# Performance work log

Measured on AMD Instinct MI355X. Metric: run time of the kernel, lower is better.

Reference implementation:

```python
import jax, jax.numpy as jnp
import numpy as np

B, S, HID = 1, 2048, 2880
NH, NKV, D = 64, 8, 64
G = NH // NKV          # GQA group size = 8
SW = 128               # sliding window
SCALE = D ** -0.5
NEG = -1e30


def rotate_half(x):
    h = x.shape[-1] // 2
    return jnp.concatenate([-x[..., h:], x[..., :h]], axis=-1)


def setup_inputs() -> dict:
    key = jax.random.key(0)
    ks = jax.random.split(key, 11)
    hidden_states = jax.random.normal(ks[0], (B, S, HID), dtype=jnp.float32)
    # RoPE tables [S, D]
    inv_freq = 1.0 / (10000.0 ** (np.arange(0, D, 2, dtype=np.float32) / D))
    freqs = np.arange(S, dtype=np.float32)[:, None] * inv_freq[None, :]
    emb = np.concatenate([freqs, freqs], axis=-1)
    cos = jnp.asarray(np.cos(emb), dtype=jnp.float32)
    sin = jnp.asarray(np.sin(emb), dtype=jnp.float32)
    std = 0.02
    wq = jax.random.normal(ks[1], (HID, NH * D), dtype=jnp.float32) * std
    bq = jax.random.normal(ks[2], (NH * D,), dtype=jnp.float32) * std
    wk = jax.random.normal(ks[3], (HID, NKV * D), dtype=jnp.float32) * std
    bk = jax.random.normal(ks[4], (NKV * D,), dtype=jnp.float32) * std
    wv = jax.random.normal(ks[5], (HID, NKV * D), dtype=jnp.float32) * std
    bv = jax.random.normal(ks[6], (NKV * D,), dtype=jnp.float32) * std
    wo = jax.random.normal(ks[7], (NH * D, HID), dtype=jnp.float32) * std
    bo = jax.random.normal(ks[8], (HID,), dtype=jnp.float32) * std
    sinks = jax.random.normal(ks[9], (NH,), dtype=jnp.float32)
    return dict(hidden_states=hidden_states, cos=cos, sin=sin, wq=wq, bq=bq,
                wk=wk, bk=bk, wv=wv, bv=bv, wo=wo, bo=bo, sinks=sinks)


def reference(hidden_states, cos, sin, wq, bq, wk, bk, wv, bv, wo, bo, sinks):
    b, s, _ = hidden_states.shape
    q = (hidden_states @ wq + bq).reshape(b, s, NH, D)
    k = (hidden_states @ wk + bk).reshape(b, s, NKV, D)
    v = (hidden_states @ wv + bv).reshape(b, s, NKV, D)
    # RoPE (rotate-half), cos/sin broadcast over batch and heads
    c = cos[None, :, None, :]
    si = sin[None, :, None, :]
    q = q * c + rotate_half(q) * si
    k = k * c + rotate_half(k) * si
    # GQA: [b, s, kv, g, d]
    qg = q.reshape(b, s, NKV, G, D)
    # scores [b, kv, g, q, s]
    scores = jnp.einsum('bqkgd,bskd->bkgqs', qg, k) * SCALE
    i = jnp.arange(s)
    allowed = (i[:, None] >= i[None, :]) & (i[:, None] - i[None, :] < SW)
    scores = jnp.where(allowed[None, None, None], scores, NEG)
    # sink softmax: per-head learnable logit added to the denominator only
    sink = sinks.reshape(NKV, G)[None, :, :, None]            # [1, kv, g, 1]
    m = jnp.maximum(scores.max(axis=-1), sink)                # [b, kv, g, q]
    e = jnp.exp(scores - m[..., None])
    denom = e.sum(axis=-1) + jnp.exp(sink - m)                # sink absorbs mass
    p = e / denom[..., None]
    attn = jnp.einsum('bkgqs,bskd->bqkgd', p, v).reshape(b, s, NH * D)
    return attn @ wo + bo
```

## Files before the change

kernel.cpp:

```cpp
#include <hip/hip_runtime.h>
#include <hip/hip_bf16.h>
#include <stdint.h>

#define S_LEN 2048
#define HID 2880
#define NH 64
#define NKV 8
#define HD 64
#define NQ (NH * HD)
#define NKVD (NKV * HD)
#define SCALE 0.125f

typedef unsigned short u16;
typedef __attribute__((ext_vector_type(8))) short short8;
typedef __attribute__((ext_vector_type(4))) float floatx4;

__device__ __forceinline__ u16 f2bf(float f) {
  union { float f; unsigned u; } x; x.f = f;
  unsigned r = x.u + 0x7fffu + ((x.u >> 16) & 1u);
  return (u16)(r >> 16);
}

__device__ __forceinline__ int xcd_swz(int orig, int nwg) {
  int q = nwg >> 3, r = nwg & 7, xcd = orig & 7, lid = orig >> 3;
  return (xcd < r ? xcd * (q + 1) : r * (q + 1) + (xcd - r) * q) + lid;
}

__device__ __forceinline__ void gl2lds16(const void* g, void* l) {
  __builtin_amdgcn_global_load_lds(
      (__attribute__((address_space(1))) unsigned int*)(uintptr_t)g,
      (__attribute__((address_space(3))) unsigned int*)(unsigned int)(uintptr_t)l,
      16, 0, 0);
}

__global__ void k_pre(const float* __restrict__ hs, u16* __restrict__ hsb,
                      const float* __restrict__ wq, const float* __restrict__ wk,
                      const float* __restrict__ wv, const float* __restrict__ wo,
                      u16* __restrict__ wqt, u16* __restrict__ wkt,
                      u16* __restrict__ wvt, u16* __restrict__ wot) {
  int b = blockIdx.x;
  const int ncv = (S_LEN * HID / 4) / 256;
  if (b < ncv) {
    int i = b * 256 + threadIdx.x;
    float4 v = ((const float4*)hs)[i];
    ushort4 o;
    o.x = f2bf(v.x); o.y = f2bf(v.y); o.z = f2bf(v.z); o.w = f2bf(v.w);
    *(ushort4*)(hsb + (size_t)i * 4) = o;
    return;
  }
  b -= ncv;
  __shared__ float tile[32][33];
  const int nwq = (NQ / 32) * (HID / 32);
  const int nwkv = (NKVD / 32) * (HID / 32);
  const float* in; u16* out; int R, C, bx, by;
  if (b < nwq) {
    in = wq; out = wqt; R = HID; C = NQ;
    int nx = NQ / 32; bx = (b % nx) * 32; by = (b / nx) * 32;
  } else if (b < nwq + nwkv) {
    b -= nwq; in = wk; out = wkt; R = HID; C = NKVD;
    int nx = NKVD / 32; bx = (b % nx) * 32; by = (b / nx) * 32;
  } else if (b < nwq + 2 * nwkv) {
    b -= nwq + nwkv; in = wv; out = wvt; R = HID; C = NKVD;
    int nx = NKVD / 32; bx = (b % nx) * 32; by = (b / nx) * 32;
  } else {
    b -= nwq + 2 * nwkv; in = wo; out = wot; R = NQ; C = HID;
    int nx = HID / 32; bx = (b % nx) * 32; by = (b / nx) * 32;
  }
  int tx = threadIdx.x & 31, ty = threadIdx.x >> 5;
#pragma unroll
  for (int i = 0; i < 4; ++i)
    tile[ty + i * 8][tx] = in[(long)(by + ty + i * 8) * C + bx + tx];
  __syncthreads();
#pragma unroll
  for (int i = 0; i < 4; ++i)
    out[(long)(bx + ty + i * 8) * R + by + tx] = f2bf(tile[tx][ty + i * 8]);
}

__device__ __forceinline__ void gemm_tile8(const u16* __restrict__ Abase, int lda,
                                           const u16* __restrict__ Bbase, int ldb,
                                           int kloop, floatx4 acc[2][4]) {
  __shared__ __align__(16) u16 As[3][128][32];
  __shared__ __align__(16) u16 Bs[3][128][32];
  const int t = threadIdx.x;
  const int w = t >> 6, l = t & 63;
  const int srow = w * 16 + (l >> 2);
  const int scol = (((l & 3) ^ ((l >> 3) & 3))) * 8;
  const int wr = (w >> 1) * 32, wc = (w & 1) * 64;
  const int fr = l & 15;
  const int fk8 = (((l >> 4) ^ ((l >> 1) & 3))) * 8;
  floatx4 zero = {0.f, 0.f, 0.f, 0.f};
#pragma unroll
  for (int i = 0; i < 2; ++i)
#pragma unroll
    for (int j = 0; j < 4; ++j) acc[i][j] = zero;

  const u16* Ar = Abase + (long)srow * lda + scol;
  const u16* Br = Bbase + (long)srow * ldb + scol;

#define STAGE8(buf, kt) do {                             \
    long ko_ = (long)(kt) * 32;                          \
    gl2lds16(Ar + ko_, &As[buf][w * 16][0]);             \
    gl2lds16(Br + ko_, &Bs[buf][w * 16][0]);             \
  } while (0)

  const int nk = kloop >> 5;
  STAGE8(0, 0);
  STAGE8(1, 1);
  int cur = 0, nxt = 1, fut = 2;
  for (int kt = 0; kt < nk; ++kt) {
    if (kt + 1 < nk) { asm volatile("s_waitcnt vmcnt(2)" ::: "memory"); }
    else             { asm volatile("s_waitcnt vmcnt(0)" ::: "memory"); }
    asm volatile("s_barrier" ::: "memory");
    if (kt + 2 < nk) STAGE8(fut, kt + 2);
    short8 af[2], bf8[4];
#pragma unroll
    for (int i = 0; i < 2; ++i) af[i] = *(const short8*)&As[cur][wr + i * 16 + fr][fk8];
#pragma unroll
    for (int j = 0; j < 4; ++j) bf8[j] = *(const short8*)&Bs[cur][wc + j * 16 + fr][fk8];
#pragma unroll
    for (int i = 0; i < 2; ++i)
#pragma unroll
      for (int j = 0; j < 4; ++j)
        acc[i][j] = __builtin_amdgcn_mfma_f32_16x16x32_bf16(af[i], bf8[j], acc[i][j], 0, 0, 0);
    int tmp = cur; cur = nxt; nxt = fut; fut = tmp;
  }
#undef STAGE8
}

__global__ __launch_bounds__(512) void k_gemm_qkv(
    const u16* __restrict__ hsb, const u16* __restrict__ wqt,
    const u16* __restrict__ wkt, const u16* __restrict__ wvt,
    const float* __restrict__ bq, const float* __restrict__ bk, const float* __restrict__ bv,
    const float* __restrict__ cosb, const float* __restrict__ sinb,
    u16* __restrict__ qbuf, u16* __restrict__ kbuf, u16* __restrict__ vtbuf) {
  int xcd = blockIdx.x & 7, lid = blockIdx.x >> 3;
  int bm = ((xcd & 1) * 8 + (lid & 7)) * 128;
  int bn = ((xcd >> 1) * 10 + (lid >> 3)) * 128;
  const u16* Bt; const float* bias;
  if (bn < NQ)              { Bt = wqt + (long)bn * HID;               bias = bq + bn; }
  else if (bn < NQ + NKVD)  { Bt = wkt + (long)(bn - NQ) * HID;        bias = bk + (bn - NQ); }
  else                      { Bt = wvt + (long)(bn - NQ - NKVD) * HID; bias = bv + (bn - NQ - NKVD); }
  floatx4 acc[2][4];
  gemm_tile8(hsb + (long)bm * HID, HID, Bt, HID, HID, acc);
  int t = threadIdx.x, w = t >> 6, l = t & 63;
  int wr = (w >> 1) * 32, wc = (w & 1) * 64, fr = l & 15, fq = (l >> 4) * 4;
  if (bn < NQ + NKVD) {
    int ng0 = bn + wc;
    u16* hbase;
    if (ng0 < NQ) hbase = qbuf + (long)(ng0 >> 6) * S_LEN * HD;
    else          hbase = kbuf + (long)((ng0 - NQ) >> 6) * S_LEN * HD;
#pragma unroll
    for (int i = 0; i < 2; ++i)
#pragma unroll
      for (int r = 0; r < 4; ++r) {
        int srow = bm + wr + i * 16 + fq + r;
        const float* crow = cosb + (long)srow * HD;
        const float* srw  = sinb + (long)srow * HD;
#pragma unroll
        for (int j = 0; j < 2; ++j) {
          int dlo = j * 16 + fr;
          float c  = crow[dlo];
          float si = srw[dlo];
          float xl = acc[i][j][r]     + bias[wc + j * 16 + fr];
          float xh = acc[i][j + 2][r] + bias[wc + (j + 2) * 16 + fr];
          hbase[(long)srow * HD + dlo]      = f2bf(xl * c - xh * si);
          hbase[(long)srow * HD + dlo + 32] = f2bf(xh * c + xl * si);
        }
      }
  } else {
#pragma unroll
    for (int i = 0; i < 2; ++i)
#pragma unroll
      for (int j = 0; j < 4; ++j) {
        int ncol = wc + j * 16 + fr;
        int n3 = bn + ncol - NQ - NKVD;
        float bsv = bias[ncol];
#pragma unroll
        for (int r = 0; r < 4; ++r) {
          int srow = bm + wr + i * 16 + fq + r;
          vtbuf[(long)(n3 >> 6) * HD * S_LEN + (long)(n3 & 63) * S_LEN + srow] =
              f2bf(acc[i][j][r] + bsv);
        }
      }
  }
}

__global__ __launch_bounds__(256) void k_attn(
    const u16* __restrict__ qb, const u16* __restrict__ kb, const u16* __restrict__ vtb,
    const float* __restrict__ sinks, u16* __restrict__ ao) {
  __shared__ __align__(16) u16 Kl[192][72];
  __shared__ __align__(16) u16 Vl[64][200];
  int t = threadIdx.x;
  int h = blockIdx.y, kvh = h >> 3;
  int qs = blockIdx.x * 64;
  int kstart = qs - 128;
  const u16* kbase = kb + (long)kvh * S_LEN * HD;
  const u16* vbase = vtb + (long)kvh * HD * S_LEN;
#pragma unroll
  for (int it = 0; it < 6; ++it) {
    int idx = t + it * 256;
    int c = idx >> 3, dc = (idx & 7) * 8;
    int j = kstart + c;
    short8 v = {0, 0, 0, 0, 0, 0, 0, 0};
    if (j >= 0) v = *(const short8*)(kbase + (long)j * HD + dc);
    *(short8*)&Kl[c][dc] = v;
  }
#pragma unroll
  for (int it = 0; it < 6; ++it) {
    int idx = t + it * 256;
    int d = idx / 24, c8 = idx % 24;
    int c = c8 * 8;
    int j = kstart + c;
    short8 v = {0, 0, 0, 0, 0, 0, 0, 0};
    if (j >= 0) v = *(const short8*)(vbase + (long)d * S_LEN + j);
    *(short8*)&Vl[d][c] = v;
  }
  __syncthreads();

  int w = t >> 6, l = t & 63;
  int fr = l & 15, fk8 = (l >> 4) * 8, fq = (l >> 4) * 4;
  const u16* qrow = qb + (long)h * S_LEN * HD + (long)(qs + w * 16 + fr) * HD;
  short8 a0 = *(const short8*)(qrow + fk8);
  short8 a1 = *(const short8*)(qrow + 32 + fk8);
  floatx4 sc[12];
#pragma unroll
  for (int ct = 0; ct < 12; ++ct) {
    floatx4 z = {0.f, 0.f, 0.f, 0.f};
    short8 b0 = *(const short8*)&Kl[ct * 16 + fr][fk8];
    short8 b1 = *(const short8*)&Kl[ct * 16 + fr][32 + fk8];
    z = __builtin_amdgcn_mfma_f32_16x16x32_bf16(a0, b0, z, 0, 0, 0);
    z = __builtin_amdgcn_mfma_f32_16x16x32_bf16(a1, b1, z, 0, 0, 0);
    sc[ct] = z;
  }
  __syncthreads();

  u16* Pw = &Kl[0][0] + w * 16 * 200;
  float snk = sinks[h];
#pragma unroll
  for (int r = 0; r < 4; ++r) {
    int rloc = w * 16 + fq + r;
    int cmin = rloc + 1;
    int jmin = 128 - qs;
    if (jmin > cmin) cmin = jmin;
    int cmax = rloc + 128;
    float vals[12];
    float mx = snk;
#pragma unroll
    for (int ct = 0; ct < 12; ++ct) {
      int c = ct * 16 + fr;
      float v = (c >= cmin && c <= cmax) ? sc[ct][r] * SCALE : -1e30f;
      vals[ct] = v;
      mx = fmaxf(mx, v);
    }
#pragma unroll
    for (int m = 1; m < 16; m <<= 1) mx = fmaxf(mx, __shfl_xor(mx, m));
    float e[12], sum = 0.f;
#pragma unroll
    for (int ct = 0; ct < 12; ++ct) { e[ct] = __expf(vals[ct] - mx); sum += e[ct]; }
#pragma unroll
    for (int m = 1; m < 16; m <<= 1) sum += __shfl_xor(sum, m);
    sum += __expf(snk - mx);
    float inv = 1.f / sum;
#pragma unroll
    for (int ct = 0; ct < 12; ++ct)
      Pw[(fq + r) * 200 + ct * 16 + fr] = f2bf(e[ct] * inv);
  }
  __syncthreads();

  floatx4 o[4];
  floatx4 zero = {0.f, 0.f, 0.f, 0.f};
#pragma unroll
  for (int cd = 0; cd < 4; ++cd) o[cd] = zero;
#pragma unroll
  for (int kk = 0; kk < 6; ++kk) {
    short8 pa = *(const short8*)(Pw + fr * 200 + kk * 32 + fk8);
#pragma unroll
    for (int cd = 0; cd < 4; ++cd) {
      short8 bv8 = *(const short8*)&Vl[cd * 16 + fr][kk * 32 + fk8];
      o[cd] = __builtin_amdgcn_mfma_f32_16x16x32_bf16(pa, bv8, o[cd], 0, 0, 0);
    }
  }
#pragma unroll
  for (int cd = 0; cd < 4; ++cd)
#pragma unroll
    for (int r = 0; r < 4; ++r) {
      int srow = qs + w * 16 + fq + r;
      ao[(long)srow * NQ + h * HD + cd * 16 + fr] = f2bf(o[cd][r]);
    }
}

__global__ __launch_bounds__(256) void k_gemm_out(
    const u16* __restrict__ attn, const u16* __restrict__ wot,
    const float* __restrict__ bo, float* __restrict__ out) {
  __shared__ __align__(16) u16 As[2][128][64];
  __shared__ __align__(16) u16 Bs[2][128][64];
  const int t = threadIdx.x;
  const int w = t >> 6, l = t & 63;
  const int sr = l >> 3;
  const int ss = ((l & 7) ^ sr) * 8;
  const int wr = (w >> 1) * 64, wc = (w & 1) * 64;
  const int fr = l & 15, g = l >> 4, fq = g * 4;
  const int fsw = fr & 7;

  int sw = xcd_swz(blockIdx.x, gridDim.x);
  int bm = (sw & 15) * 128, bn = (sw >> 4) * 128;
  const u16* Ar = attn + (long)bm * NQ;
  const u16* Br = wot + (long)bn * NQ;

  floatx4 acc[4][4];
  floatx4 zero = {0.f, 0.f, 0.f, 0.f};
#pragma unroll
  for (int i = 0; i < 4; ++i)
#pragma unroll
    for (int j = 0; j < 4; ++j) acc[i][j] = zero;

#define OSTAGE(buf, kt) do {                                          \
    long ko_ = (long)(kt) * 64 + ss;                                  \
    _Pragma("unroll")                                                 \
    for (int c8 = 0; c8 < 4; ++c8) {                                  \
      int r0 = w * 32 + c8 * 8;                                       \
      gl2lds16(Ar + (long)(r0 + sr) * NQ + ko_, &As[buf][r0][0]);     \
      gl2lds16(Br + (long)(r0 + sr) * NQ + ko_, &Bs[buf][r0][0]);     \
    } } while (0)

  const int nk = NQ >> 6;
  OSTAGE(0, 0);
  for (int kt = 0; kt < nk; ++kt) {
    const int cb = kt & 1;
    asm volatile("s_waitcnt vmcnt(0)" ::: "memory");
    asm volatile("s_barrier" ::: "memory");
    if (kt + 1 < nk) OSTAGE(cb ^ 1, kt + 1);
    short8 af[4][2], bf8[4][2];
#pragma unroll
    for (int i = 0; i < 4; ++i)
#pragma unroll
      for (int kk = 0; kk < 2; ++kk)
        af[i][kk] = *(const short8*)&As[cb][wr + i * 16 + fr][((kk * 4 + g) ^ fsw) * 8];
#pragma unroll
    for (int j = 0; j < 4; ++j)
#pragma unroll
      for (int kk = 0; kk < 2; ++kk)
        bf8[j][kk] = *(const short8*)&Bs[cb][wc + j * 16 + fr][((kk * 4 + g) ^ fsw) * 8];
#pragma unroll
    for (int i = 0; i < 4; ++i)
#pragma unroll
      for (int j = 0; j < 4; ++j)
#pragma unroll
        for (int kk = 0; kk < 2; ++kk)
          acc[i][j] = __builtin_amdgcn_mfma_f32_16x16x32_bf16(
              af[i][kk], bf8[j][kk], acc[i][j], 0, 0, 0);
  }
#undef OSTAGE

  int fqe = (l >> 4) * 4;
#pragma unroll
  for (int i = 0; i < 4; ++i)
#pragma unroll
    for (int j = 0; j < 4; ++j) {
      int ng = bn + wc + j * 16 + fr;
      if (ng >= HID) continue;
      float bsv = bo[ng];
#pragma unroll
      for (int r = 0; r < 4; ++r) {
        int srow = bm + wr + i * 16 + fqe + r;
        out[(long)srow * HID + ng] = acc[i][j][r] + bsv;
      }
    }
}

extern "C" void kernel_launch(void* const* d_in, const int* in_sizes, int n_in,
                              void* d_out, int out_size, void* d_ws, size_t ws_size,
                              hipStream_t stream) {
  const float* hs    = (const float*)d_in[0];
  const float* cosb  = (const float*)d_in[1];
  const float* sinb  = (const float*)d_in[2];
  const float* wq    = (const float*)d_in[3];
  const float* bq    = (const float*)d_in[4];
  const float* wk    = (const float*)d_in[5];
  const float* bk    = (const float*)d_in[6];
  const float* wv    = (const float*)d_in[7];
  const float* bv    = (const float*)d_in[8];
  const float* wo    = (const float*)d_in[9];
  const float* bo    = (const float*)d_in[10];
  const float* sinks = (const float*)d_in[11];
  float* out = (float*)d_out;

  char* p = (char*)d_ws;
  u16* hsb   = (u16*)p; p += (size_t)S_LEN * HID * 2;
  u16* wqt   = (u16*)p; p += (size_t)NQ * HID * 2;
  u16* wkt   = (u16*)p; p += (size_t)NKVD * HID * 2;
  u16* wvt   = (u16*)p; p += (size_t)NKVD * HID * 2;
  u16* wot   = (u16*)p; p += (size_t)2944 * NQ * 2;
  u16* qbuf  = (u16*)p; p += (size_t)NH * S_LEN * HD * 2;
  u16* kbuf  = (u16*)p; p += (size_t)NKV * S_LEN * HD * 2;
  u16* vtbuf = (u16*)p; p += (size_t)NKV * HD * S_LEN * 2;
  u16* abuf  = (u16*)p; p += (size_t)S_LEN * NQ * 2;

  const int npre = (S_LEN * HID / 4) / 256 +
                   (NQ / 32) * (HID / 32) * 2 + (NKVD / 32) * (HID / 32) * 2;
  k_pre<<<npre, 256, 0, stream>>>(hs, hsb, wq, wk, wv, wo, wqt, wkt, wvt, wot);
  k_gemm_qkv<<<(NQ + 2 * NKVD) / 128 * (S_LEN / 128), 512, 0, stream>>>(
      hsb, wqt, wkt, wvt, bq, bk, bv, cosb, sinb, qbuf, kbuf, vtbuf);
  k_attn<<<dim3(S_LEN / 64, NH), 256, 0, stream>>>(qbuf, kbuf, vtbuf, sinks, abuf);
  k_gemm_out<<<23 * 16, 256, 0, stream>>>(abuf, wot, bo, out);
}
```

Baseline: 202.9 us.

## Switch QKV GEMM to 64-wide K tiles with double buffering

Changes the QKV projection GEMM core from a 3-stage pipeline with 32-element K steps to a 2-stage pipeline with 64-element K steps. Each iteration issues two MFMAs per output fragment and does half as many barriers and waits. The aim is to cut per-iteration synchronization and loop overhead. The trade-off is a shallower prefetch (wait vmcnt(0) every step), which may expose global load latency. HID=2880 is divisible by 64, so the tail is handled.

```diff
diff --git a/kernel.cpp b/kernel.cpp
--- a/kernel.cpp
+++ b/kernel.cpp
@@ -76,55 +76,65 @@
     out[(long)(bx + ty + i * 8) * R + by + tx] = f2bf(tile[tx][ty + i * 8]);
 }
 
-__device__ __forceinline__ void gemm_tile8(const u16* __restrict__ Abase, int lda,
-                                           const u16* __restrict__ Bbase, int ldb,
-                                           int kloop, floatx4 acc[2][4]) {
-  __shared__ __align__(16) u16 As[3][128][32];
-  __shared__ __align__(16) u16 Bs[3][128][32];
+__device__ __forceinline__ void gemm_tile8_64(const u16* __restrict__ Abase, int lda,
+                                              const u16* __restrict__ Bbase, int ldb,
+                                              int kloop, floatx4 acc[2][4]) {
+  __shared__ __align__(16) u16 As[2][128][64];
+  __shared__ __align__(16) u16 Bs[2][128][64];
   const int t = threadIdx.x;
   const int w = t >> 6, l = t & 63;
-  const int srow = w * 16 + (l >> 2);
-  const int scol = (((l & 3) ^ ((l >> 3) & 3))) * 8;
+  const int sr = l >> 3;
+  const int ss = ((l & 7) ^ sr) * 8;
   const int wr = (w >> 1) * 32, wc = (w & 1) * 64;
-  const int fr = l & 15;
-  const int fk8 = (((l >> 4) ^ ((l >> 1) & 3))) * 8;
+  const int fr = l & 15, g = l >> 4;
+  const int fsw = fr & 7;
   floatx4 zero = {0.f, 0.f, 0.f, 0.f};
 #pragma unroll
   for (int i = 0; i < 2; ++i)
 #pragma unroll
     for (int j = 0; j < 4; ++j) acc[i][j] = zero;
 
-  const u16* Ar = Abase + (long)srow * lda + scol;
-  const u16* Br = Bbase + (long)srow * ldb + scol;
-
-#define STAGE8(buf, kt) do {                             \
-    long ko_ = (long)(kt) * 32;                          \
-    gl2lds16(Ar + ko_, &As[buf][w * 16][0]);             \
-    gl2lds16(Br + ko_, &Bs[buf][w * 16][0]);             \
+  const u16* Ar0 = Abase + (long)(w * 16 + sr) * lda + ss;
+  const u16* Ar1 = Abase + (long)(w * 16 + 8 + sr) * lda + ss;
+  const u16* Br0 = Bbase + (long)(w * 16 + sr) * ldb + ss;
+  const u16* Br1 = Bbase + (long)(w * 16 + 8 + sr) * ldb + ss;
+
+#define STAGE64(buf, kt) do {                            \
+    long ko_ = (long)(kt) * 64;                          \
+    gl2lds16(Ar0 + ko_, &As[buf][w * 16][0]);            \
+    gl2lds16(Ar1 + ko_, &As[buf][w * 16 + 8][0]);        \
+    gl2lds16(Br0 + ko_, &Bs[buf][w * 16][0]);            \
+    gl2lds16(Br1 + ko_, &Bs[buf][w * 16 + 8][0]);        \
   } while (0)
 
-  const int nk = kloop >> 5;
-  STAGE8(0, 0);
-  STAGE8(1, 1);
-  int cur = 0, nxt = 1, fut = 2;
+  const int nk = kloop >> 6;
+  STAGE64(0, 0);
   for (int kt = 0; kt < nk; ++kt) {
-    if (kt + 1 < nk) { asm volatile("s_waitcnt vmcnt(2)" ::: "memory"); }
-    else             { asm volatile("s_waitcnt vmcnt(0)" ::: "memory"); }
+    const int cb = kt & 1;
+    asm volatile("s_waitcnt vmcnt(0)" ::: "memory");
     asm volatile("s_barrier" ::: "memory");
-    if (kt + 2 < nk) STAGE8(fut, kt + 2);
-    short8 af[2], bf8[4];
-#pragma unroll
-    for (int i = 0; i < 2; ++i) af[i] = *(const short8*)&As[cur][wr + i * 16 + fr][fk8];
-#pragma unroll
-    for (int j = 0; j < 4; ++j) bf8[j] = *(const short8*)&Bs[cur][wc + j * 16 + fr][fk8];
+    if (kt + 1 < nk) STAGE64(cb ^ 1, kt + 1);
+    short8 af[2][2], bf8[4][2];
 #pragma unroll
     for (int i = 0; i < 2; ++i)
 #pragma unroll
+      for (int kk = 0; kk < 2; ++kk)
+        af[i][kk] = *(const short8*)&As[cb][wr + i * 16 + fr][((kk * 4 + g) ^ fsw) * 8];
+#pragma unroll
+    for (int j = 0; j < 4; ++j)
+#pragma unroll
+      for (int kk = 0; kk < 2; ++kk)
+        bf8[j][kk] = *(const short8*)&Bs[cb][wc + j * 16 + fr][((kk * 4 + g) ^ fsw) * 8];
+#pragma unroll
+    for (int i = 0; i < 2; ++i)
+#pragma unroll
       for (int j = 0; j < 4; ++j)
-        acc[i][j] = __builtin_amdgcn_mfma_f32_16x16x32_bf16(af[i], bf8[j], acc[i][j], 0, 0, 0);
-    int tmp = cur; cur = nxt; nxt = fut; fut = tmp;
-  }
-#undef STAGE8
+#pragma unroll
+        for (int kk = 0; kk < 2; ++kk)
+          acc[i][j] = __builtin_amdgcn_mfma_f32_16x16x32_bf16(
+              af[i][kk], bf8[j][kk], acc[i][j], 0, 0, 0);
+  }
+#undef STAGE64
 }
 
 __global__ __launch_bounds__(512) void k_gemm_qkv(
@@ -141,7 +151,7 @@
   else if (bn < NQ + NKVD)  { Bt = wkt + (long)(bn - NQ) * HID;        bias = bk + (bn - NQ); }
   else                      { Bt = wvt + (long)(bn - NQ - NKVD) * HID; bias = bv + (bn - NQ - NKVD); }
   floatx4 acc[2][4];
-  gemm_tile8(hsb + (long)bm * HID, HID, Bt, HID, HID, acc);
+  gemm_tile8_64(hsb + (long)bm * HID, HID, Bt, HID, HID, acc);
   int t = threadIdx.x, w = t >> 6, l = t & 63;
   int wr = (w >> 1) * 32, wc = (w & 1) * 64, fr = l & 15, fq = (l >> 4) * 4;
   if (bn < NQ + NKVD) {
@@ -299,7 +309,7 @@
   const int sr = l >> 3;
   const int ss = ((l & 7) ^ sr) * 8;
   const int wr = (w >> 1) * 64, wc = (w & 1) * 64;
-  const int fr = l & 15, g = l >> 4, fq = g * 4;
+  const int fr = l & 15, g = l >> 4;
   const int fsw = fr & 7;
 
   int sw = xcd_swz(blockIdx.x, gridDim.x);
```

After: 194.3 us. -4.2%, faster.
